# Kernel tuning notes

Measured on AMD Instinct MI355X. Metric: run time of the kernel, lower is better.

The kernel has to match this reference:

```python
import jax, jax.numpy as jnp
import numpy as np

ROPE_DIM = 64
ROPE_THETA = 10000.0
SLIDING_WINDOW = 1024
_K_MASK = jnp.finfo(jnp.bfloat16).min


def _pos_embeddings(positions, head_dim, rope_theta):
    # positions: [B, T] -> sin, cos: [B, T, head_dim]
    fraction = jnp.arange(0, head_dim, 2, dtype=jnp.float32) / head_dim
    inv_freq = 1.0 / (rope_theta ** fraction)
    sinusoid = jnp.einsum('BT,k->BTk', positions.astype(jnp.float32), inv_freq,
                          precision=jax.lax.Precision.HIGHEST)
    sin = jnp.sin(sinusoid); cos = jnp.cos(sinusoid)
    return jnp.concatenate([sin, sin], -1), jnp.concatenate([cos, cos], -1)


def _rotate_half(x):
    x1, x2 = x[..., :x.shape[-1] // 2], x[..., x.shape[-1] // 2:]
    return jnp.concatenate([-x2, x1], -1)


def _apply_rope_partial(x, sin, cos, rope_dim):
    x_rope, x_nope = x[..., :rope_dim], x[..., rope_dim:]
    sin = sin[:, :, None, :]; cos = cos[:, :, None, :]
    x_rope = x_rope * cos + _rotate_half(x_rope) * sin
    return jnp.concatenate([x_rope, x_nope], -1).astype(x.dtype)


def setup_inputs() -> dict:
    key = jax.random.key(0)
    ks = jax.random.split(key, 6)
    B, T, D = 2, 2048, 2048
    N, K, H, Hv = 16, 4, 128, 128
    S = 2048  # cache size
    sc = 0.02
    return {
        'x': jax.random.normal(ks[0], (B, T, D), jnp.float32),
        'wq': jax.random.normal(ks[1], (D, N, H), jnp.float32) * sc,
        'wk': jax.random.normal(ks[2], (D, K, H), jnp.float32) * sc,
        'wv': jax.random.normal(ks[3], (D, K, Hv), jnp.float32) * sc,
        'wo': jax.random.normal(ks[4], (N, Hv, D), jnp.float32) * sc,
        'sink_bias': jnp.zeros((N,), jnp.float32),
        'k_cache': jnp.zeros((B, S, K, H), jnp.float32),
        'v_cache': jnp.zeros((B, S, K, Hv), jnp.float32),
        'segment_ids': jnp.ones((B, T), jnp.int32),
        'cur_ind': 0,
        'start_ind': -jnp.ones((B,), jnp.int32),
    }


def reference(x, wq, wk, wv, wo, sink_bias, k_cache, v_cache,
              segment_ids, cur_ind, start_ind):
    B, T, D = x.shape
    N, H = wq.shape[1], wq.shape[2]
    K, Hv = wk.shape[1], wv.shape[2]
    n_rep = N // K
    scaling = H ** -0.5
    cur_ind = jnp.asarray(cur_ind, jnp.int32)

    q = jnp.einsum('BTD,DNH->BTNH', x, wq)
    k = jnp.einsum('BSD,DKH->BSKH', x, wk)
    v = jnp.einsum('BSD,DKV->BSKV', x, wv)

    # left pads / positions from segment ids
    left_pads = jnp.sum(jnp.cumsum(segment_ids != 0, axis=-1) == 0, -1).astype(jnp.int32)
    start = jnp.where(start_ind < 0, left_pads, start_ind)
    pos = jax.vmap(lambda row: jnp.where(row != 0,
                                         jnp.arange(T, dtype=jnp.int32) - jnp.argmax(row).astype(jnp.int32),
                                         2 ** 30))(segment_ids) + cur_ind
    sin, cos = _pos_embeddings(pos, ROPE_DIM, ROPE_THETA)
    q = _apply_rope_partial(q, sin, cos, ROPE_DIM)
    k = _apply_rope_partial(k, sin, cos, ROPE_DIM)

    # KV cache append
    kc = jax.lax.dynamic_update_slice(k_cache, k, (0, cur_ind, 0, 0))
    vc = jax.lax.dynamic_update_slice(v_cache, v, (0, cur_ind, 0, 0))
    S = kc.shape[1]

    # GQA repeat
    kr = jnp.repeat(kc[:, :, :, None, :], n_rep, axis=3).reshape(B, S, N, H)
    vr = jnp.repeat(vc[:, :, :, None, :], n_rep, axis=3).reshape(B, S, N, Hv)

    logits = jnp.einsum('BTNH,BSNH->BTNS', q, kr) * scaling

    q_pos = cur_ind + jnp.arange(T, dtype=jnp.int32)[None, :] - start[:, None]
    ts = jnp.arange(S, dtype=jnp.int32)
    kv_seg = (ts[None, :] >= start[:, None]) & (ts[None, :] < cur_ind + T)
    k_pos = ts[None, :] - start[:, None]
    causal = k_pos[:, None, :] <= q_pos[:, :, None]
    seg_mask = kv_seg[:, None, :] == segment_ids[:, :, None]
    window = k_pos[:, None, :] >= q_pos[:, :, None] - (SLIDING_WINDOW - 1)
    final_mask = causal & seg_mask & window  # [B, T, S]
    logits = jnp.where(final_mask[:, :, None, :], logits, _K_MASK)

    # attention sink bias: extra softmax slot per head
    sink = jnp.broadcast_to(sink_bias[None, None, :, None], (B, T, N, 1))
    logits = jnp.concatenate([logits, sink], axis=-1)
    weights = jax.nn.softmax(logits.astype(jnp.float32), axis=-1).astype(logits.dtype)
    weights = weights[..., :-1]

    attn = jnp.einsum('BTNS,BSNV->BTNV', weights, vr)
    return jnp.einsum('BTNV,NVD->BTD', attn, wo)
```

## Files before the change

### kernel.cpp

```cpp
#include <hip/hip_runtime.h>
#include <hip/hip_bf16.h>
#include <stdint.h>

#define BB 2
#define TT 2048
#define DD 2048
#define NHQ 16
#define KH 4
#define HD 128
#define SS 2048
#define WINDOW 1024
#define M2FIX 12.0f
#define QSC_LOG2E 0.12751751f
#define LOG2E 1.4426950408889634f
#define NLOG2F 0.4152410118609203f

typedef __attribute__((ext_vector_type(8))) short bf16x8;
typedef __attribute__((ext_vector_type(4))) float f32x4;
typedef __attribute__((ext_vector_type(16))) float f32x16;

#define MFMA16(a, b, c) __builtin_amdgcn_mfma_f32_16x16x32_bf16(a, b, c, 0, 0, 0)
#define MFMA32(a, b, c) __builtin_amdgcn_mfma_f32_32x32x16_bf16(a, b, c, 0, 0, 0)

__device__ __forceinline__ ushort f2bf(float f) {
  uint32_t u = __float_as_uint(f);
  u += 0x7FFF + ((u >> 16) & 1);
  return (ushort)(u >> 16);
}
__device__ __forceinline__ ushort f2bf_trunc(float f) {
  return (ushort)(__float_as_uint(f) >> 16);
}
__device__ __forceinline__ float bf2f(ushort h) {
  return __uint_as_float(((uint32_t)h) << 16);
}

__device__ __forceinline__ void async_copy16(const ushort* g, ushort* l) {
  __builtin_amdgcn_global_load_lds(
      (const __attribute__((address_space(1))) uint32_t*)g,
      (__attribute__((address_space(3))) uint32_t*)l, 16, 0, 0);
}

__device__ __forceinline__ void tr_tile(const float* __restrict__ in,
                                        ushort* __restrict__ out,
                                        int C, int ldo, int cx, int cy) {
  __shared__ float tile[32][33];
  int tx = threadIdx.x & 31, ty = threadIdx.x >> 5;
  int r0 = cy * 32, c0 = cx * 32;
#pragma unroll
  for (int k = 0; k < 4; k++)
    tile[ty + k * 8][tx] = in[(size_t)(r0 + ty + k * 8) * C + c0 + tx];
  __syncthreads();
#pragma unroll
  for (int k = 0; k < 4; k++)
    out[(size_t)(c0 + ty + k * 8) * ldo + r0 + tx] = f2bf(tile[tx][ty + k * 8]);
}

__global__ void prep_fused(const float* __restrict__ x, const float* __restrict__ wq,
                           const float* __restrict__ wk, const float* __restrict__ wv,
                           const float* __restrict__ wo, const int* __restrict__ seg,
                           const int* __restrict__ start_ind, ushort* __restrict__ xb,
                           ushort* __restrict__ WcatT, ushort* __restrict__ WoT,
                           int* __restrict__ meta) {
  int bz = blockIdx.x;
  int tid = threadIdx.x;
  if (bz < 2) {
    __shared__ int red[256];
    int b = bz;
    int first = TT;
    for (int t = tid; t < TT; t += 256)
      if (seg[b * TT + t] != 0) first = min(first, t);
    red[tid] = first;
    __syncthreads();
    for (int s = 128; s > 0; s >>= 1) {
      if (tid < s) red[tid] = min(red[tid], red[tid + s]);
      __syncthreads();
    }
    if (tid == 0) {
      int fi = red[0];
      int st = start_ind[b] < 0 ? fi : start_ind[b];
      meta[b * 2 + 0] = st;
      meta[b * 2 + 1] = (fi >= TT) ? 0 : fi;
    }
    return;
  }
  bz -= 2;
  if (bz < 2048) {
#pragma unroll
    for (int p = 0; p < 4; p++) {
      int i = bz * 1024 + p * 256 + tid;
      float4 v = ((const float4*)x)[i];
      ushort4 o;
      o.x = f2bf(v.x); o.y = f2bf(v.y); o.z = f2bf(v.z); o.w = f2bf(v.w);
      ((ushort4*)xb)[i] = o;
    }
    return;
  }
  bz -= 2048;
  if (bz < 4096) { tr_tile(wq, WcatT, 2048, 2048, bz & 63, bz >> 6); return; }
  bz -= 4096;
  if (bz < 1024) { tr_tile(wk, WcatT + (size_t)2048 * 2048, 512, 2048, bz & 15, bz >> 4); return; }
  bz -= 1024;
  if (bz < 1024) { tr_tile(wv, WcatT + (size_t)2560 * 2048, 512, 2048, bz & 15, bz >> 4); return; }
  bz -= 1024;
  tr_tile(wo, WoT, 2048, 2048, bz & 63, bz >> 6);
}

__global__ void transpose_v(const ushort* __restrict__ in, ushort* __restrict__ out) {
  __shared__ ushort tile[32][33];
  int mtx = blockIdx.z;
  in  += (size_t)mtx * SS * HD;
  out += (size_t)mtx * SS * HD;
  int tx = threadIdx.x & 31, ty = threadIdx.x >> 5;
  int s0 = blockIdx.x * 32, h0 = blockIdx.y * 32;
#pragma unroll
  for (int k = 0; k < 4; k++)
    tile[ty + k * 8][tx] = in[(size_t)(s0 + ty + k * 8) * HD + h0 + tx];
  __syncthreads();
#pragma unroll
  for (int k = 0; k < 4; k++) {
    int h = h0 + ty + k * 8;
    int s = s0 + tx;
    int cit = (s & 63) >> 3;
    int sout = (s & ~63) | ((cit ^ (h & 7)) << 3) | (s & 7);
    out[(size_t)h * SS + sout] = tile[tx][ty + k * 8];
  }
}

__global__ __launch_bounds__(256) void gemm_qkv(const ushort* __restrict__ A,
                                                const ushort* __restrict__ Bt,
                                                const int* __restrict__ seg,
                                                const int* __restrict__ cur_p,
                                                const int* __restrict__ meta,
                                                ushort* __restrict__ qa,
                                                ushort* __restrict__ ka,
                                                ushort* __restrict__ va) {
  const int K = DD;
  __shared__ ushort As[128 * 64];
  __shared__ ushort Bs[128 * 64];
  __shared__ float posf_s[128];
  int tid = threadIdx.x;
  int lane = tid & 63, wave = tid >> 6;
  int wr = wave >> 1, wc = wave & 1;
  int orig = blockIdx.y * 24 + blockIdx.x;
  int wid = (orig & 7) * 96 + (orig >> 3);
  int by = wid / 24, bx = wid - by * 24;
  int row0 = by * 128, col0 = bx * 128;
  int l31 = lane & 31, khalf = lane >> 5, lx8 = l31 & 7;
  int cur = cur_p[0];

  if (tid < 128) {
    int m = row0 + tid;
    int bb = m >> 11, t = m & 2047;
    int segv = seg[m];
    int first = meta[bb * 2 + 1];
    posf_s[tid] = (segv != 0) ? (float)(t - first + cur) : 1073741824.0f;
  }

  f32x16 acc[2][2];
#pragma unroll
  for (int i = 0; i < 2; i++)
#pragma unroll
    for (int j = 0; j < 2; j++)
#pragma unroll
      for (int e = 0; e < 16; e++) acc[i][j][e] = 0.f;

  int srow = tid >> 3, scol = tid & 7;
  int ssw = (scol ^ (srow & 7)) * 8;
  const ushort* Ag = A  + (size_t)(row0 + srow) * K + ssw;
  const ushort* Bg = Bt + (size_t)(col0 + srow) * K + ssw;
  ushort* AsD = As + tid * 8;
  ushort* BsD = Bs + tid * 8;

  for (int kc = 0; kc < K; kc += 64) {
    __syncthreads();
#pragma unroll
    for (int p = 0; p < 4; p++)
      async_copy16(Ag + kc + (size_t)(p * 32) * K, AsD + p * 2048);
#pragma unroll
    for (int p = 0; p < 4; p++)
      async_copy16(Bg + kc + (size_t)(p * 32) * K, BsD + p * 2048);
    __syncthreads();
#pragma unroll
    for (int ks = 0; ks < 4; ks++) {
      bf16x8 af[2], bfm[2];
      int ch = (ks * 2 + khalf) ^ lx8;
#pragma unroll
      for (int i = 0; i < 2; i++)
        af[i] = *(const bf16x8*)(As + (wr * 64 + i * 32 + l31) * 64 + ch * 8);
#pragma unroll
      for (int j = 0; j < 2; j++)
        bfm[j] = *(const bf16x8*)(Bs + (wc * 64 + j * 32 + l31) * 64 + ch * 8);
#pragma unroll
      for (int i = 0; i < 2; i++)
#pragma unroll
        for (int j = 0; j < 2; j++)
          acc[i][j] = MFMA32(af[i], bfm[j], acc[i][j]);
    }
  }

  int cb0 = col0 + wc * 64;
  int region = (cb0 < 2048) ? 0 : (cb0 < 2560 ? 1 : 2);
  bool ropehalf = ((cb0 & 64) == 0) && (region <= 1);
  int hbase = cb0 & 64;
  float invf = exp2f(-NLOG2F * (float)l31);

#pragma unroll
  for (int i = 0; i < 2; i++) {
#pragma unroll
    for (int reg = 0; reg < 16; reg++) {
      int rloc = wr * 64 + i * 32 + (reg & 3) + 8 * (reg >> 2) + 4 * khalf;
      int m = row0 + rloc;
      int b = m >> 11, t = m & 2047;
      float v0 = acc[i][0][reg], v1 = acc[i][1][reg];
      if (ropehalf) {
        float posf = posf_s[rloc];
        float sn, cs;
        __sincosf(posf * invf, &sn, &cs);
        float n0 = v0 * cs - v1 * sn;
        v1 = v1 * cs + v0 * sn;
        v0 = n0;
      }
      if (region == 0) {
        int head = cb0 >> 7;
        size_t base = ((size_t)(b * NHQ + head) * TT + t) * HD + hbase;
        qa[base + l31]      = f2bf(v0 * QSC_LOG2E);
        qa[base + 32 + l31] = f2bf(v1 * QSC_LOG2E);
      } else if (region == 1) {
        int head = (cb0 - 2048) >> 7;
        size_t rowbase = ((size_t)(b * KH + head) * SS + t) * HD;
        int sw = t & 7;
        int c0x = hbase + l31, c1x = hbase + 32 + l31;
        ka[rowbase + ((((c0x >> 3) ^ sw) << 3) | (c0x & 7))] = f2bf(v0);
        ka[rowbase + ((((c1x >> 3) ^ sw) << 3) | (c1x & 7))] = f2bf(v1);
      } else {
        int head = (cb0 - 2560) >> 7;
        size_t base = ((size_t)(b * KH + head) * SS + t) * HD + hbase;
        va[base + l31]      = f2bf(v0);
        va[base + 32 + l31] = f2bf(v1);
      }
    }
  }
}

template <int OUT_F32>
__global__ __launch_bounds__(256) void gemm_bt(const ushort* __restrict__ A,
                                               const ushort* __restrict__ Bt,
                                               void* __restrict__ Cout,
                                               int M, int N, int K) {
  __shared__ ushort As[128 * 64];
  __shared__ ushort Bs[128 * 64];
  int tid = threadIdx.x;
  int lane = tid & 63, wave = tid >> 6;
  int wr = wave >> 1, wc = wave & 1;
  int orig = blockIdx.y * gridDim.x + blockIdx.x;
  int nwg = gridDim.x * gridDim.y;
  int cpx = nwg >> 3;
  int wid = (orig & 7) * cpx + (orig >> 3);
  int by = wid / gridDim.x, bx = wid - by * gridDim.x;
  int row0 = by * 128, col0 = bx * 128;
  int l31 = lane & 31, khalf = lane >> 5, lx8 = l31 & 7;

  f32x16 acc[2][2];
#pragma unroll
  for (int i = 0; i < 2; i++)
#pragma unroll
    for (int j = 0; j < 2; j++)
#pragma unroll
      for (int e = 0; e < 16; e++) acc[i][j][e] = 0.f;

  int srow = tid >> 3, scol = tid & 7;
  int ssw = (scol ^ (srow & 7)) * 8;
  const ushort* Ag = A  + (size_t)(row0 + srow) * K + ssw;
  const ushort* Bg = Bt + (size_t)(col0 + srow) * K + ssw;
  ushort* AsD = As + tid * 8;
  ushort* BsD = Bs + tid * 8;

  for (int kc = 0; kc < K; kc += 64) {
    __syncthreads();
#pragma unroll
    for (int p = 0; p < 4; p++)
      async_copy16(Ag + kc + (size_t)(p * 32) * K, AsD + p * 2048);
#pragma unroll
    for (int p = 0; p < 4; p++)
      async_copy16(Bg + kc + (size_t)(p * 32) * K, BsD + p * 2048);
    __syncthreads();
#pragma unroll
    for (int ks = 0; ks < 4; ks++) {
      bf16x8 af[2], bfm[2];
      int ch = (ks * 2 + khalf) ^ lx8;
#pragma unroll
      for (int i = 0; i < 2; i++)
        af[i] = *(const bf16x8*)(As + (wr * 64 + i * 32 + l31) * 64 + ch * 8);
#pragma unroll
      for (int j = 0; j < 2; j++)
        bfm[j] = *(const bf16x8*)(Bs + (wc * 64 + j * 32 + l31) * 64 + ch * 8);
#pragma unroll
      for (int i = 0; i < 2; i++)
#pragma unroll
        for (int j = 0; j < 2; j++)
          acc[i][j] = MFMA32(af[i], bfm[j], acc[i][j]);
    }
  }

#pragma unroll
  for (int i = 0; i < 2; i++)
#pragma unroll
    for (int reg = 0; reg < 16; reg++) {
      int r = row0 + wr * 64 + i * 32 + (reg & 3) + 8 * (reg >> 2) + 4 * khalf;
#pragma unroll
      for (int j = 0; j < 2; j++) {
        int c = col0 + wc * 64 + j * 32 + l31;
        float v = acc[i][j][reg];
        if (OUT_F32)
          ((float*)Cout)[(size_t)r * N + c] = v;
        else
          ((ushort*)Cout)[(size_t)r * N + c] = f2bf(v);
      }
    }
}

__global__ __launch_bounds__(256) void flash_attn(
    const ushort* __restrict__ qa, const ushort* __restrict__ ka,
    const ushort* __restrict__ vat, const float* __restrict__ sink_bias,
    const int* __restrict__ seg, const int* __restrict__ cur_p,
    const int* __restrict__ meta, ushort* __restrict__ Obuf) {
  __shared__ ushort Ks[64 * 128];
  __shared__ ushort VT[128 * 64];
  __shared__ ushort Ps[4 * 16 * 64];

  int bx = blockIdx.x;
  int u = bx & 255, v = bx >> 8;
  int combo = u & 31, j5 = u >> 5;
  int b = combo >> 4, n = combo & 15;
  int qt = (v == 0) ? j5 : (v == 1) ? (15 - j5) : (v == 2) ? (16 + j5) : (31 - j5);
  int kb = n >> 2;
  int t0 = qt * 64;
  int cur = cur_p[0];
  int start = meta[b * 2];

  int tid = threadIdx.x, lane = tid & 63, w = tid >> 6;
  int lcol = lane & 15, quad = lane >> 4, lx = lcol & 7;
  int t0w = t0 + w * 16;

  const ushort* qbase = qa + (size_t)(b * NHQ + n) * TT * HD;
  const ushort* kbase = ka + (size_t)(b * KH + kb) * SS * HD;
  const ushort* vtb   = vat + (size_t)(b * KH + kb) * HD * SS;

  bf16x8 qf[4];
  {
    const ushort* qrow = qbase + (size_t)(t0w + lcol) * HD + quad * 8;
#pragma unroll
    for (int c = 0; c < 4; c++) qf[c] = *(const bf16x8*)(qrow + c * 32);
  }

  int segq[4], trow[4];
#pragma unroll
  for (int r = 0; r < 4; r++) {
    trow[r] = t0w + quad * 4 + r;
    segq[r] = seg[b * TT + trow[r]];
  }
  int seg1 = __all(segq[0] == 1 && segq[1] == 1 && segq[2] == 1 && segq[3] == 1);

  f32x4 oacc[8], lacc;
#pragma unroll
  for (int ob = 0; ob < 8; ob++) { f32x4 z = {0.f, 0.f, 0.f, 0.f}; oacc[ob] = z; }
  { f32x4 z = {0.f, 0.f, 0.f, 0.f}; lacc = z; }

  bf16x8 ones;
#pragma unroll
  for (int e = 0; e < 8; e++) ones[e] = (short)0x3F80;

  ushort* KsD = Ks + tid * 8;
  ushort* VTD = VT + tid * 8;
  const ushort* KgT = kbase + tid * 8;
  const ushort* VgT = vtb + (size_t)(tid >> 3) * SS + (tid & 7) * 8;

  int lo = cur + t0 - (WINDOW - 1); if (lo < 0) lo = 0;
  int hi = cur + t0 + 63;           if (hi > SS - 1) hi = SS - 1;
  int ktlo = lo >> 6, kthi = hi >> 6;

  ushort* PsW = Ps + w * 1024;

  for (int kt = ktlo; kt <= kthi; kt++) {
    int ks0 = kt * 64;
    __syncthreads();
#pragma unroll
    for (int p = 0; p < 4; p++)
      async_copy16(KgT + (size_t)ks0 * 128 + p * 2048, KsD + p * 2048);
#pragma unroll
    for (int p = 0; p < 4; p++)
      async_copy16(VgT + ks0 + (size_t)p * 32 * SS, VTD + p * 2048);
    __syncthreads();

    bool active = (ks0 <= cur + t0w + 15) && (ks0 + 63 >= cur + t0w - (WINDOW - 1));
    if (active) {
      f32x4 sacc[4];
#pragma unroll
      for (int cb = 0; cb < 4; cb++) { f32x4 z = {0.f, 0.f, 0.f, 0.f}; sacc[cb] = z; }
#pragma unroll
      for (int c = 0; c < 4; c++) {
#pragma unroll
        for (int cb = 0; cb < 4; cb++) {
          bf16x8 kf = *(const bf16x8*)(Ks + (cb * 16 + lcol) * 128 +
                                       (((c * 4 + quad) ^ lx)) * 8);
          sacc[cb] = MFMA16(qf[c], kf, sacc[cb]);
        }
      }

      bool fast = seg1 && (ks0 >= start) && (ks0 + 63 <= cur + t0w) &&
                  (ks0 >= cur + t0w + 15 - (WINDOW - 1));
      if (fast) {
#pragma unroll
        for (int r = 0; r < 4; r++) {
          int row = quad * 4 + r;
#pragma unroll
          for (int cb = 0; cb < 4; cb++) {
            float p = exp2f(sacc[cb][r] - M2FIX);
            PsW[row * 64 + (((cb * 2 + (lcol >> 3)) ^ (row & 7)) * 8) + lx] = f2bf_trunc(p);
          }
        }
      } else {
        int sidx[4], kvseg[4];
#pragma unroll
        for (int cb = 0; cb < 4; cb++) {
          sidx[cb] = ks0 + cb * 16 + lcol;
          kvseg[cb] = (sidx[cb] >= start && sidx[cb] < cur + TT) ? 1 : 0;
        }
#pragma unroll
        for (int r = 0; r < 4; r++) {
          int row = quad * 4 + r;
          int qp = (segq[r] != 0) ? (cur + trow[r]) : (1 << 29);
#pragma unroll
          for (int cb = 0; cb < 4; cb++) {
            bool ok = (sidx[cb] <= qp) && (sidx[cb] >= qp - (WINDOW - 1)) &&
                      (kvseg[cb] == segq[r]);
            float p = ok ? exp2f(sacc[cb][r] - M2FIX) : 0.f;
            PsW[row * 64 + (((cb * 2 + (lcol >> 3)) ^ (row & 7)) * 8) + lx] = f2bf_trunc(p);
          }
        }
      }

#pragma unroll
      for (int c2 = 0; c2 < 2; c2++) {
        bf16x8 pf = *(const bf16x8*)(PsW + lcol * 64 + (((c2 * 4 + quad) ^ lx)) * 8);
#pragma unroll
        for (int ob = 0; ob < 8; ob++) {
          bf16x8 vf = *(const bf16x8*)(VT + (ob * 16 + lcol) * 64 +
                                       (((c2 * 4 + quad) ^ lx)) * 8);
          oacc[ob] = MFMA16(pf, vf, oacc[ob]);
        }
        lacc = MFMA16(pf, ones, lacc);
      }
    }
  }

  float sb = sink_bias[n];
#pragma unroll
  for (int r = 0; r < 4; r++) {
    float l = lacc[r] + exp2f(sb * LOG2E - M2FIX);
    float inv = 1.f / l;
    int t = trow[r];
    size_t base = ((size_t)(b * TT + t)) * (NHQ * HD) + n * HD;
#pragma unroll
    for (int ob = 0; ob < 8; ob++)
      Obuf[base + ob * 16 + lcol] = f2bf(oacc[ob][r] * inv);
  }
}

extern "C" void kernel_launch(void* const* d_in, const int* in_sizes, int n_in,
                              void* d_out, int out_size, void* d_ws, size_t ws_size,
                              hipStream_t stream) {
  const float* x  = (const float*)d_in[0];
  const float* wq = (const float*)d_in[1];
  const float* wk = (const float*)d_in[2];
  const float* wv = (const float*)d_in[3];
  const float* wo = (const float*)d_in[4];
  const float* sink = (const float*)d_in[5];
  const int* seg = (const int*)d_in[8];
  const int* cur = (const int*)d_in[9];
  const int* start_ind = (const int*)d_in[10];

  char* ws = (char*)d_ws;
  ushort* xb    = (ushort*)(ws + 0);
  ushort* WcatT = (ushort*)(ws + 16777216);
  ushort* WoT   = (ushort*)(ws + 29360128);
  ushort* qa    = (ushort*)(ws + 37748736);
  ushort* ka    = (ushort*)(ws + 54525952);
  ushort* va    = (ushort*)(ws + 58720256);
  ushort* vat   = (ushort*)(ws + 62914560);
  ushort* Obuf  = (ushort*)(ws + 67108864);
  int*    meta  = (int*)(ws + 83886080);

  prep_fused<<<12290, 256, 0, stream>>>(x, wq, wk, wv, wo, seg, start_ind,
                                        xb, WcatT, WoT, meta);
  gemm_qkv<<<dim3(24, 32), 256, 0, stream>>>(xb, WcatT, seg, cur, meta, qa, ka, va);
  transpose_v<<<dim3(64, 4, 8), 256, 0, stream>>>(va, vat);
  flash_attn<<<1024, 256, 0, stream>>>(qa, ka, vat, sink, seg, cur, meta, Obuf);
  gemm_bt<1><<<dim3(16, 32), 256, 0, stream>>>(Obuf, WoT, d_out, 4096, 2048, 2048);
}
```

Before: 307.8 us.

## Fuse V transpose into QKV GEMM epilogue and share KV tiles across GQA heads

The QKV GEMM epilogue now transposes V tiles through shared memory and writes the swizzled V^T layout directly, which removes the separate transpose_v kernel and its extra global round trip. Flash attention is remapped so each block covers one KV head, with its four waves handling the four query heads of that group over a 32-row query tile in two 16-row groups. Each K/V tile loaded into LDS is therefore reused by all heads sharing it, halving the grid and cutting K/V reload traffic. The cost is doubled accumulator registers per wave and more shared memory for P.

```diff
diff --git a/kernel.cpp b/kernel.cpp
--- a/kernel.cpp
+++ b/kernel.cpp
@@ -105,27 +105,6 @@
   tr_tile(wo, WoT, 2048, 2048, bz & 63, bz >> 6);
 }
 
-__global__ void transpose_v(const ushort* __restrict__ in, ushort* __restrict__ out) {
-  __shared__ ushort tile[32][33];
-  int mtx = blockIdx.z;
-  in  += (size_t)mtx * SS * HD;
-  out += (size_t)mtx * SS * HD;
-  int tx = threadIdx.x & 31, ty = threadIdx.x >> 5;
-  int s0 = blockIdx.x * 32, h0 = blockIdx.y * 32;
-#pragma unroll
-  for (int k = 0; k < 4; k++)
-    tile[ty + k * 8][tx] = in[(size_t)(s0 + ty + k * 8) * HD + h0 + tx];
-  __syncthreads();
-#pragma unroll
-  for (int k = 0; k < 4; k++) {
-    int h = h0 + ty + k * 8;
-    int s = s0 + tx;
-    int cit = (s & 63) >> 3;
-    int sout = (s & ~63) | ((cit ^ (h & 7)) << 3) | (s & 7);
-    out[(size_t)h * SS + sout] = tile[tx][ty + k * 8];
-  }
-}
-
 __global__ __launch_bounds__(256) void gemm_qkv(const ushort* __restrict__ A,
                                                 const ushort* __restrict__ Bt,
                                                 const int* __restrict__ seg,
@@ -133,11 +112,12 @@
                                                 const int* __restrict__ meta,
                                                 ushort* __restrict__ qa,
                                                 ushort* __restrict__ ka,
-                                                ushort* __restrict__ va) {
+                                                ushort* __restrict__ vat) {
   const int K = DD;
-  __shared__ ushort As[128 * 64];
-  __shared__ ushort Bs[128 * 64];
-  __shared__ float posf_s[128];
+  __shared__ ushort SH[16640];
+  ushort* As = SH;
+  ushort* Bs = SH + 8192;
+  float* posf_s = (float*)(SH + 16384);
   int tid = threadIdx.x;
   int lane = tid & 63, wave = tid >> 6;
   int wr = wave >> 1, wc = wave & 1;
@@ -200,44 +180,66 @@
 
   int cb0 = col0 + wc * 64;
   int region = (cb0 < 2048) ? 0 : (cb0 < 2560 ? 1 : 2);
-  bool ropehalf = ((cb0 & 64) == 0) && (region <= 1);
-  int hbase = cb0 & 64;
-  float invf = exp2f(-NLOG2F * (float)l31);
-
-#pragma unroll
-  for (int i = 0; i < 2; i++) {
-#pragma unroll
-    for (int reg = 0; reg < 16; reg++) {
-      int rloc = wr * 64 + i * 32 + (reg & 3) + 8 * (reg >> 2) + 4 * khalf;
-      int m = row0 + rloc;
-      int b = m >> 11, t = m & 2047;
-      float v0 = acc[i][0][reg], v1 = acc[i][1][reg];
-      if (ropehalf) {
-        float posf = posf_s[rloc];
-        float sn, cs;
-        __sincosf(posf * invf, &sn, &cs);
-        float n0 = v0 * cs - v1 * sn;
-        v1 = v1 * cs + v0 * sn;
-        v0 = n0;
+
+  if (region <= 1) {
+    bool ropehalf = ((cb0 & 64) == 0);
+    int hbase = cb0 & 64;
+    float invf = exp2f(-NLOG2F * (float)l31);
+#pragma unroll
+    for (int i = 0; i < 2; i++) {
+#pragma unroll
+      for (int reg = 0; reg < 16; reg++) {
+        int rloc = wr * 64 + i * 32 + (reg & 3) + 8 * (reg >> 2) + 4 * khalf;
+        int m = row0 + rloc;
+        int b = m >> 11, t = m & 2047;
+        float v0 = acc[i][0][reg], v1 = acc[i][1][reg];
+        if (ropehalf) {
+          float posf = posf_s[rloc];
+          float sn, cs;
+          __sincosf(posf * invf, &sn, &cs);
+          float n0 = v0 * cs - v1 * sn;
+          v1 = v1 * cs + v0 * sn;
+          v0 = n0;
+        }
+        if (region == 0) {
+          int head = cb0 >> 7;
+          size_t base = ((size_t)(b * NHQ + head) * TT + t) * HD + hbase;
+          qa[base + l31]      = f2bf(v0 * QSC_LOG2E);
+          qa[base + 32 + l31] = f2bf(v1 * QSC_LOG2E);
+        } else {
+          int head = (cb0 - 2048) >> 7;
+          size_t rowbase = ((size_t)(b * KH + head) * SS + t) * HD;
+          int sw = t & 7;
+          int c0x = hbase + l31, c1x = hbase + 32 + l31;
+          ka[rowbase + ((((c0x >> 3) ^ sw) << 3) | (c0x & 7))] = f2bf(v0);
+          ka[rowbase + ((((c1x >> 3) ^ sw) << 3) | (c1x & 7))] = f2bf(v1);
+        }
       }
-      if (region == 0) {
-        int head = cb0 >> 7;
-        size_t base = ((size_t)(b * NHQ + head) * TT + t) * HD + hbase;
-        qa[base + l31]      = f2bf(v0 * QSC_LOG2E);
-        qa[base + 32 + l31] = f2bf(v1 * QSC_LOG2E);
-      } else if (region == 1) {
-        int head = (cb0 - 2048) >> 7;
-        size_t rowbase = ((size_t)(b * KH + head) * SS + t) * HD;
-        int sw = t & 7;
-        int c0x = hbase + l31, c1x = hbase + 32 + l31;
-        ka[rowbase + ((((c0x >> 3) ^ sw) << 3) | (c0x & 7))] = f2bf(v0);
-        ka[rowbase + ((((c1x >> 3) ^ sw) << 3) | (c1x & 7))] = f2bf(v1);
-      } else {
-        int head = (cb0 - 2560) >> 7;
-        size_t base = ((size_t)(b * KH + head) * SS + t) * HD + hbase;
-        va[base + l31]      = f2bf(v0);
-        va[base + 32 + l31] = f2bf(v1);
+    }
+  } else {
+    __syncthreads();
+    ushort* TB = SH;
+    int hbase = wc * 64;
+#pragma unroll
+    for (int i = 0; i < 2; i++)
+#pragma unroll
+      for (int reg = 0; reg < 16; reg++) {
+        int rloc = wr * 64 + i * 32 + (reg & 3) + 8 * (reg >> 2) + 4 * khalf;
+        int h0 = hbase + l31, h1 = hbase + 32 + l31;
+        TB[h0 * 128 + (rloc ^ ((h0 & 15) << 3))] = f2bf(acc[i][0][reg]);
+        TB[h1 * 128 + (rloc ^ ((h1 & 15) << 3))] = f2bf(acc[i][1][reg]);
       }
+    __syncthreads();
+    int headv = (col0 - 2560) >> 7;
+    int bv = row0 >> 11;
+    ushort* vout = vat + (size_t)(bv * KH + headv) * HD * SS + (row0 & 2047);
+#pragma unroll
+    for (int pass = 0; pass < 8; pass++) {
+      int idx = pass * 256 + tid;
+      int h = idx >> 4, cc = idx & 15;
+      int s64 = cc >> 3, c = cc & 7;
+      bf16x8 vd = *(const bf16x8*)(TB + h * 128 + (s64 ^ ((h >> 3) & 1)) * 64 + c * 8);
+      *(bf16x8*)(vout + (size_t)h * SS + s64 * 64 + c * 8) = vd;
     }
   }
 }
@@ -326,45 +328,47 @@
     const int* __restrict__ meta, ushort* __restrict__ Obuf) {
   __shared__ ushort Ks[64 * 128];
   __shared__ ushort VT[128 * 64];
-  __shared__ ushort Ps[4 * 16 * 64];
-
-  int bx = blockIdx.x;
-  int u = bx & 255, v = bx >> 8;
-  int combo = u & 31, j5 = u >> 5;
-  int b = combo >> 4, n = combo & 15;
-  int qt = (v == 0) ? j5 : (v == 1) ? (15 - j5) : (v == 2) ? (16 + j5) : (31 - j5);
-  int kb = n >> 2;
-  int t0 = qt * 64;
+  __shared__ ushort Ps[4 * 2048];
+
+  int bxx = blockIdx.x;
+  int kb = bxx & 3, b = (bxx >> 2) & 1;
+  int jr = bxx >> 3;
+  int j32 = (jr & 1) ? (63 - (jr >> 1)) : (jr >> 1);
+  int t0 = j32 * 32;
   int cur = cur_p[0];
   int start = meta[b * 2];
 
   int tid = threadIdx.x, lane = tid & 63, w = tid >> 6;
+  int n = kb * 4 + w;
   int lcol = lane & 15, quad = lane >> 4, lx = lcol & 7;
-  int t0w = t0 + w * 16;
 
   const ushort* qbase = qa + (size_t)(b * NHQ + n) * TT * HD;
   const ushort* kbase = ka + (size_t)(b * KH + kb) * SS * HD;
   const ushort* vtb   = vat + (size_t)(b * KH + kb) * HD * SS;
 
-  bf16x8 qf[4];
-  {
-    const ushort* qrow = qbase + (size_t)(t0w + lcol) * HD + quad * 8;
-#pragma unroll
-    for (int c = 0; c < 4; c++) qf[c] = *(const bf16x8*)(qrow + c * 32);
-  }
-
-  int segq[4], trow[4];
-#pragma unroll
-  for (int r = 0; r < 4; r++) {
-    trow[r] = t0w + quad * 4 + r;
-    segq[r] = seg[b * TT + trow[r]];
-  }
-  int seg1 = __all(segq[0] == 1 && segq[1] == 1 && segq[2] == 1 && segq[3] == 1);
-
-  f32x4 oacc[8], lacc;
-#pragma unroll
-  for (int ob = 0; ob < 8; ob++) { f32x4 z = {0.f, 0.f, 0.f, 0.f}; oacc[ob] = z; }
-  { f32x4 z = {0.f, 0.f, 0.f, 0.f}; lacc = z; }
+  bf16x8 qf[2][4];
+  int segq[2][4], trow[2][4], seg1[2];
+#pragma unroll
+  for (int g = 0; g < 2; g++) {
+    const ushort* qrow = qbase + (size_t)(t0 + g * 16 + lcol) * HD + quad * 8;
+#pragma unroll
+    for (int c = 0; c < 4; c++) qf[g][c] = *(const bf16x8*)(qrow + c * 32);
+#pragma unroll
+    for (int r = 0; r < 4; r++) {
+      trow[g][r] = t0 + g * 16 + quad * 4 + r;
+      segq[g][r] = seg[b * TT + trow[g][r]];
+    }
+    seg1[g] = __all(segq[g][0] == 1 && segq[g][1] == 1 &&
+                    segq[g][2] == 1 && segq[g][3] == 1);
+  }
+
+  f32x4 oacc[2][8], lacc[2];
+#pragma unroll
+  for (int g = 0; g < 2; g++) {
+#pragma unroll
+    for (int ob = 0; ob < 8; ob++) { f32x4 z = {0.f, 0.f, 0.f, 0.f}; oacc[g][ob] = z; }
+    f32x4 z = {0.f, 0.f, 0.f, 0.f}; lacc[g] = z;
+  }
 
   bf16x8 ones;
 #pragma unroll
@@ -376,10 +380,8 @@
   const ushort* VgT = vtb + (size_t)(tid >> 3) * SS + (tid & 7) * 8;
 
   int lo = cur + t0 - (WINDOW - 1); if (lo < 0) lo = 0;
-  int hi = cur + t0 + 63;           if (hi > SS - 1) hi = SS - 1;
+  int hi = cur + t0 + 31;           if (hi > SS - 1) hi = SS - 1;
   int ktlo = lo >> 6, kthi = hi >> 6;
-
-  ushort* PsW = Ps + w * 1024;
 
   for (int kt = ktlo; kt <= kthi; kt++) {
     int ks0 = kt * 64;
@@ -392,8 +394,13 @@
       async_copy16(VgT + ks0 + (size_t)p * 32 * SS, VTD + p * 2048);
     __syncthreads();
 
-    bool active = (ks0 <= cur + t0w + 15) && (ks0 + 63 >= cur + t0w - (WINDOW - 1));
-    if (active) {
+#pragma unroll
+    for (int g = 0; g < 2; g++) {
+      int t0g = t0 + g * 16;
+      bool active = (ks0 <= cur + t0g + 15) && (ks0 + 63 >= cur + t0g - (WINDOW - 1));
+      if (!active) continue;
+
+      ushort* PsG = Ps + w * 2048 + g * 1024;
       f32x4 sacc[4];
 #pragma unroll
       for (int cb = 0; cb < 4; cb++) { f32x4 z = {0.f, 0.f, 0.f, 0.f}; sacc[cb] = z; }
@@ -403,12 +410,12 @@
         for (int cb = 0; cb < 4; cb++) {
           bf16x8 kf = *(const bf16x8*)(Ks + (cb * 16 + lcol) * 128 +
                                        (((c * 4 + quad) ^ lx)) * 8);
-          sacc[cb] = MFMA16(qf[c], kf, sacc[cb]);
+          sacc[cb] = MFMA16(qf[g][c], kf, sacc[cb]);
         }
       }
 
-      bool fast = seg1 && (ks0 >= start) && (ks0 + 63 <= cur + t0w) &&
-                  (ks0 >= cur + t0w + 15 - (WINDOW - 1));
+      bool fast = seg1[g] && (ks0 >= start) && (ks0 + 63 <= cur + t0g) &&
+                  (ks0 >= cur + t0g + 15 - (WINDOW - 1));
       if (fast) {
 #pragma unroll
         for (int r = 0; r < 4; r++) {
@@ -416,7 +423,7 @@
 #pragma unroll
           for (int cb = 0; cb < 4; cb++) {
             float p = exp2f(sacc[cb][r] - M2FIX);
-            PsW[row * 64 + (((cb * 2 + (lcol >> 3)) ^ (row & 7)) * 8) + lx] = f2bf_trunc(p);
+            PsG[row * 64 + (((cb * 2 + (lcol >> 3)) ^ (row & 7)) * 8) + lx] = f2bf_trunc(p);
           }
         }
       } else {
@@ -429,41 +436,44 @@
 #pragma unroll
         for (int r = 0; r < 4; r++) {
           int row = quad * 4 + r;
-          int qp = (segq[r] != 0) ? (cur + trow[r]) : (1 << 29);
+          int qp = (segq[g][r] != 0) ? (cur + trow[g][r]) : (1 << 29);
 #pragma unroll
           for (int cb = 0; cb < 4; cb++) {
             bool ok = (sidx[cb] <= qp) && (sidx[cb] >= qp - (WINDOW - 1)) &&
-                      (kvseg[cb] == segq[r]);
+                      (kvseg[cb] == segq[g][r]);
             float p = ok ? exp2f(sacc[cb][r] - M2FIX) : 0.f;
-            PsW[row * 64 + (((cb * 2 + (lcol >> 3)) ^ (row & 7)) * 8) + lx] = f2bf_trunc(p);
+            PsG[row * 64 + (((cb * 2 + (lcol >> 3)) ^ (row & 7)) * 8) + lx] = f2bf_trunc(p);
           }
         }
       }
 
 #pragma unroll
       for (int c2 = 0; c2 < 2; c2++) {
-        bf16x8 pf = *(const bf16x8*)(PsW + lcol * 64 + (((c2 * 4 + quad) ^ lx)) * 8);
+        bf16x8 pf = *(const bf16x8*)(PsG + lcol * 64 + (((c2 * 4 + quad) ^ lx)) * 8);
 #pragma unroll
         for (int ob = 0; ob < 8; ob++) {
           bf16x8 vf = *(const bf16x8*)(VT + (ob * 16 + lcol) * 64 +
                                        (((c2 * 4 + quad) ^ lx)) * 8);
-          oacc[ob] = MFMA16(pf, vf, oacc[ob]);
-        }
-        lacc = MFMA16(pf, ones, lacc);
+          oacc[g][ob] = MFMA16(pf, vf, oacc[g][ob]);
+        }
+        lacc[g] = MFMA16(pf, ones, lacc[g]);
       }
     }
   }
 
   float sb = sink_bias[n];
 #pragma unroll
-  for (int r = 0; r < 4; r++) {
-    float l = lacc[r] + exp2f(sb * LOG2E - M2FIX);
-    float inv = 1.f / l;
-    int t = trow[r];
-    size_t base = ((size_t)(b * TT + t)) * (NHQ * HD) + n * HD;
-#pragma unroll
-    for (int ob = 0; ob < 8; ob++)
-      Obuf[base + ob * 16 + lcol] = f2bf(oacc[ob][r] * inv);
+  for (int g = 0; g < 2; g++) {
+#pragma unroll
+    for (int r = 0; r < 4; r++) {
+      float l = lacc[g][r] + exp2f(sb * LOG2E - M2FIX);
+      float inv = 1.f / l;
+      int t = trow[g][r];
+      size_t base = ((size_t)(b * TT + t)) * (NHQ * HD) + n * HD;
+#pragma unroll
+      for (int ob = 0; ob < 8; ob++)
+        Obuf[base + ob * 16 + lcol] = f2bf(oacc[g][ob][r] * inv);
+    }
   }
 }
 
@@ -486,15 +496,13 @@
   ushort* WoT   = (ushort*)(ws + 29360128);
   ushort* qa    = (ushort*)(ws + 37748736);
   ushort* ka    = (ushort*)(ws + 54525952);
-  ushort* va    = (ushort*)(ws + 58720256);
   ushort* vat   = (ushort*)(ws + 62914560);
   ushort* Obuf  = (ushort*)(ws + 67108864);
   int*    meta  = (int*)(ws + 83886080);
 
   prep_fused<<<12290, 256, 0, stream>>>(x, wq, wk, wv, wo, seg, start_ind,
                                         xb, WcatT, WoT, meta);
-  gemm_qkv<<<dim3(24, 32), 256, 0, stream>>>(xb, WcatT, seg, cur, meta, qa, ka, va);
-  transpose_v<<<dim3(64, 4, 8), 256, 0, stream>>>(va, vat);
-  flash_attn<<<1024, 256, 0, stream>>>(qa, ka, vat, sink, seg, cur, meta, Obuf);
+  gemm_qkv<<<dim3(24, 32), 256, 0, stream>>>(xb, WcatT, seg, cur, meta, qa, ka, vat);
+  flash_attn<<<512, 256, 0, stream>>>(qa, ka, vat, sink, seg, cur, meta, Obuf);
   gemm_bt<1><<<dim3(16, 32), 256, 0, stream>>>(Obuf, WoT, d_out, 4096, 2048, 2048);
 }
```

New measurement: 333.7 us. 1.08x slower.
